# Kernel optimization log

Measured on AMD Instinct MI355X. Metric: run time of the kernel, lower is better.

## Reference

```python
import jax, jax.numpy as jnp
import numpy as np

NUM_HEADS = 16
NUM_KV_HEADS = 4
HEAD_DIM = 64
ROPE_BASE = 10000.0


def _rope(x, pos0):
    # x: [b, s, n, h_d]; interleaved-pair RoPE (torchtune RotaryPositionalEmbeddings)
    b, s, n, hd = x.shape
    half = hd // 2
    inv_freq = 1.0 / (ROPE_BASE ** (jnp.arange(0, hd, 2, dtype=jnp.float32) / hd))  # [half]
    t = jnp.arange(s, dtype=jnp.float32) + pos0                                      # [s]
    freqs = t[:, None] * inv_freq[None, :]                                           # [s, half]
    cos = jnp.cos(freqs)[None, :, None, :].astype(x.dtype)
    sin = jnp.sin(freqs)[None, :, None, :].astype(x.dtype)
    xr = x.reshape(b, s, n, half, 2)
    x1, x2 = xr[..., 0], xr[..., 1]
    o1 = x1 * cos - x2 * sin
    o2 = x1 * sin + x2 * cos
    return jnp.stack([o1, o2], axis=-1).reshape(b, s, n, hd)


def setup_inputs() -> dict:
    key = jax.random.key(0)
    k1, k2, k3 = jax.random.split(key, 3)
    b, s, d = 2, 2048, 1024
    qkv_dim = (NUM_HEADS + 2 * NUM_KV_HEADS) * HEAD_DIM  # 1536
    x = jax.random.normal(k1, (b, s, d), dtype=jnp.float32)
    Wqkv = jax.random.normal(k2, (d, qkv_dim), dtype=jnp.float32) * (d ** -0.5)
    Wo = jax.random.normal(k3, (d, d), dtype=jnp.float32) * (d ** -0.5)
    return {"x": x, "Wqkv": Wqkv, "Wo": Wo, "curr_pos": 0}


def reference(x, Wqkv, Wo, curr_pos):
    b, s, d = x.shape
    n_h, n_kv, hd = NUM_HEADS, NUM_KV_HEADS, HEAD_DIM
    q_per_kv = n_h // n_kv
    total_qkv = q_per_kv + 2

    # fused QKV projection then split per kv group
    qkv = (x @ Wqkv).reshape(b, s, n_kv, total_qkv, hd)
    q = qkv[:, :, :, :q_per_kv]            # [b, s, n_kv, q_per_kv, hd]
    k = qkv[:, :, :, q_per_kv:q_per_kv + 1]  # [b, s, n_kv, 1, hd]
    v = qkv[:, :, :, q_per_kv + 1:]          # [b, s, n_kv, 1, hd]

    # GQA expand k/v to match query heads, then flatten heads
    k = jnp.broadcast_to(k, (b, s, n_kv, q_per_kv, hd))
    v = jnp.broadcast_to(v, (b, s, n_kv, q_per_kv, hd))
    q = q.reshape(b, s, n_h, hd)
    k = k.reshape(b, s, n_h, hd)
    v = v.reshape(b, s, n_h, hd)

    # RoPE on q and k
    q = _rope(q, curr_pos)
    k = _rope(k, curr_pos)

    # causal SDPA (kv_cache is None -> is_causal=True, mask=None, dropout=0)
    scale = 1.0 / jnp.sqrt(jnp.asarray(hd, dtype=x.dtype))
    scores = jnp.einsum('bqhd,bkhd->bhqk', q, k) * scale  # [b, n_h, s, s]
    causal = jnp.tril(jnp.ones((s, s), dtype=bool))
    scores = jnp.where(causal[None, None], scores, jnp.finfo(scores.dtype).min)
    attn = jax.nn.softmax(scores, axis=-1)
    out = jnp.einsum('bhqk,bkhd->bqhd', attn, v).reshape(b, s, n_h * hd)
    return out @ Wo
```

## Files before the change

kernel.cpp:

```cpp
#include <hip/hip_runtime.h>
#include <hip/hip_bf16.h>

typedef __attribute__((ext_vector_type(8))) short bf16x8;
typedef __attribute__((ext_vector_type(4))) short bf16x4;
typedef __attribute__((ext_vector_type(4))) float f32x4;
typedef __attribute__((ext_vector_type(16))) float f32x16;
typedef unsigned short u16;
typedef unsigned int u32;

#define NH 16
#define NKV 4
#define HD 64
#define BB 2
#define SS 2048
#define DD 1024
#define QKVD 1536

#define QSCALE 0.18033688011112f
#define MBIAS  -12.0f

template<int V> struct IntC { static constexpr int value = V; };

__device__ __forceinline__ u16 f2b(float f){
  __hip_bfloat16 h = __float2bfloat16(f);
  u16 u; __builtin_memcpy(&u, &h, 2); return u;
}
__device__ __forceinline__ float b2f(u32 u){
  u <<= 16; float f; __builtin_memcpy(&f, &u, 4); return f;
}
__device__ __forceinline__ float exp2fast(float x){
#if __has_builtin(__builtin_amdgcn_exp2f)
  return __builtin_amdgcn_exp2f(x);
#else
  return exp2f(x);
#endif
}

__device__ __forceinline__ void gload16(const void* g, void* l){
  __builtin_amdgcn_global_load_lds((const __attribute__((address_space(1))) void*)g,
                                   (__attribute__((address_space(3))) void*)l, 16, 0, 0);
}

__global__ __launch_bounds__(256) void prep1(const float* __restrict__ x,
                                             u16* __restrict__ Xb,
                                             const float* __restrict__ Wqkv,
                                             u16* __restrict__ WqkvT,
                                             const float* __restrict__ Wo,
                                             u16* __restrict__ WoT){
  __shared__ u16 tile[64][65];
  const int bid = blockIdx.x;
  if (bid < 4096){
    int idx = (bid * 256 + threadIdx.x) * 4;
    float4 v = *(const float4*)(x + idx);
    u32 lo = (u32)f2b(v.x) | ((u32)f2b(v.y) << 16);
    u32 hi = (u32)f2b(v.z) | ((u32)f2b(v.w) << 16);
    *(uint2*)(Xb + idx) = make_uint2(lo, hi);
    return;
  }
  const float* in; u16* outT; int K, N, n0, k0;
  if (bid < 4480){
    int id = bid - 4096; in = Wqkv; outT = WqkvT; K = 1024; N = 1536;
    n0 = (id % 24) * 64; k0 = (id / 24) * 64;
  } else {
    int id = bid - 4480; in = Wo; outT = WoT; K = 1024; N = 1024;
    n0 = (id % 16) * 64; k0 = (id / 16) * 64;
  }
  int cr = threadIdx.x >> 6, cc = threadIdx.x & 63;
#pragma unroll
  for (int rr = 0; rr < 16; rr++){
    int row = rr * 4 + cr;
    tile[row][cc] = f2b(in[(size_t)(k0 + row) * N + n0 + cc]);
  }
  __syncthreads();
#pragma unroll
  for (int rr = 0; rr < 16; rr++){
    int row = rr * 4 + cr;
    outT[(size_t)(n0 + row) * K + k0 + cc] = tile[cc][row];
  }
}

template<int TN, typename OT>
__global__ __launch_bounds__(256) void gemm_db(const __hip_bfloat16* __restrict__ A,
                                               const __hip_bfloat16* __restrict__ BT,
                                               OT* __restrict__ C,
                                               int M, int N, int K){
  constexpr int NW = TN / 32;
  constexpr int ABYTES = 128 * 128;
  constexpr int BBYTES = TN * 128;
  __shared__ __align__(16) char smem[2][ABYTES + BBYTES];
  const int ntn = N / TN;
  int bid = blockIdx.x;
  const int cpx = gridDim.x >> 3;
  bid = (bid & 7) * cpx + (bid >> 3);
  const int tm = bid / ntn, tn = bid % ntn;
  const int m0 = tm << 7, n0 = tn * TN;
  const int lane = threadIdx.x & 63, w = threadIdx.x >> 6;
  const int g = lane >> 4, i = lane & 15;
  const int wr = w >> 1, wc = w & 1;
  f32x4 acc[4][NW] = {};
  const int lrow = lane >> 3;
  const int lcol = ((lane & 7) ^ lrow) * 8;
  const __hip_bfloat16* ga = A  + (size_t)(m0 + w * 32 + lrow) * K + lcol;
  const __hip_bfloat16* gb = BT + (size_t)(n0 + w * 8 + lrow) * K + lcol;
  const int xr = (i & 7) << 4;

  auto stage = [&](int buf, int kt){
    char* As = smem[buf];
    char* Bs = As + ABYTES;
#pragma unroll
    for (int h = 0; h < 4; h++)
      gload16(ga + kt + (size_t)(h * 8) * K, As + w * 4096 + h * 1024);
#pragma unroll
    for (int h = 0; h < NW; h++)
      gload16(gb + kt + (size_t)(h * 32) * K, Bs + (h * 4 + w) * 1024);
  };

  stage(0, 0);
  asm volatile("s_waitcnt vmcnt(0)");
  __syncthreads();
  int cur = 0;
  for (int kt = 0; kt < K; kt += 64){
    if (kt + 64 < K) stage(cur ^ 1, kt + 64);
    const char* As = smem[cur];
    const char* Bs = As + ABYTES;
    bf16x8 af[2][4], bfr[2][NW];
#pragma unroll
    for (int kh = 0; kh < 2; kh++){
#pragma unroll
      for (int x = 0; x < 4; x++)
        af[kh][x] = *(const bf16x8*)(As + (wr * 64 + x * 16 + i) * 128 + ((kh * 64 + g * 16) ^ xr));
#pragma unroll
      for (int n = 0; n < NW; n++)
        bfr[kh][n] = *(const bf16x8*)(Bs + (wc * (TN / 2) + n * 16 + i) * 128 + ((kh * 64 + g * 16) ^ xr));
    }
    __builtin_amdgcn_s_setprio(1);
#pragma unroll
    for (int kh = 0; kh < 2; kh++)
#pragma unroll
      for (int mi = 0; mi < 4; mi++)
#pragma unroll
        for (int ni = 0; ni < NW; ni++)
          acc[mi][ni] = __builtin_amdgcn_mfma_f32_16x16x32_bf16(af[kh][mi], bfr[kh][ni], acc[mi][ni], 0, 0, 0);
    __builtin_amdgcn_s_setprio(0);
    asm volatile("s_waitcnt vmcnt(0)");
    __syncthreads();
    cur ^= 1;
  }
#pragma unroll
  for (int mi = 0; mi < 4; mi++)
#pragma unroll
    for (int ni = 0; ni < NW; ni++){
      size_t base = (size_t)(m0 + wr * 64 + mi * 16 + g * 4) * N + n0 + wc * (TN / 2) + ni * 16 + i;
#pragma unroll
      for (int r = 0; r < 4; r++){
        float v = acc[mi][ni][r];
        if constexpr (sizeof(OT) == 2) C[base + (size_t)r * N] = (OT)f2b(v);
        else                           C[base + (size_t)r * N] = v;
      }
    }
}

__global__ __launch_bounds__(256) void prep2(const u16* __restrict__ qkv,
                                             const int* __restrict__ posp,
                                             u16* __restrict__ Qr,
                                             u16* __restrict__ Kr,
                                             u16* __restrict__ Vt){
  __shared__ u16 tile[64][65];
  const int bid = blockIdx.x;
  if (bid < 10240){
    int bx = bid & 255, h20 = (bid >> 8) % 20, bi = bid / 5120;
    int t = bx * 256 + threadIdx.x;
    int p = t & 31, si = t >> 5;
    int kvh = h20 / 5, slot = h20 - kvh * 5;
    const u16* src = qkv + (size_t)(bi * SS + si) * QKVD + (kvh * 6 + slot) * 64 + 2 * p;
    u32 pair = *(const u32*)src;
    float x1 = b2f(pair & 0xffffu), x2 = b2f(pair >> 16);
    int pos0 = posp[0];
    float inv_freq = exp2fast(-(float)p * 0.4152410118609203f);
    float ang = (float)(si + pos0) * inv_freq;
    float sn, cs;
    sincosf(ang, &sn, &cs);
    float o1 = x1 * cs - x2 * sn;
    float o2 = x1 * sn + x2 * cs;
    u16* dst;
    if (slot == 4){
      dst = Kr + ((size_t)(bi * NKV + kvh) * SS + si) * 64 + 2 * p;
    } else {
      o1 *= QSCALE; o2 *= QSCALE;
      dst = Qr + ((size_t)(bi * NH + kvh * 4 + slot) * SS + si) * 64 + 2 * p;
    }
    *(u32*)dst = (u32)f2b(o1) | ((u32)f2b(o2) << 16);
    return;
  }
  int id2 = bid - 10240;
  int st0 = (id2 & 31) * 64;
  int bkv = id2 >> 5;
  int bi = bkv >> 2, kvh = bkv & 3;
  int cr = threadIdx.x >> 6, cc = threadIdx.x & 63;
  const u16* src = qkv + (size_t)(bi * SS + st0) * QKVD + (kvh * 6 + 5) * 64;
#pragma unroll
  for (int rr = 0; rr < 16; rr++){
    int row = rr * 4 + cr;
    tile[row][cc] = src[(size_t)row * QKVD + cc];
  }
  __syncthreads();
  u16* dst = Vt + (size_t)bkv * 64 * SS + st0;
#pragma unroll
  for (int rr = 0; rr < 16; rr++){
    int row = rr * 4 + cr;
    dst[(size_t)row * SS + cc] = tile[cc][row];
  }
}

__global__ __launch_bounds__(256) void attn_fwd(const __hip_bfloat16* __restrict__ Qr,
                                                const __hip_bfloat16* __restrict__ Kr,
                                                const __hip_bfloat16* __restrict__ Vt,
                                                u16* __restrict__ Ao){
  __shared__ __align__(16) char smem[2][16384];
  const int blk = blockIdx.x;
  const int qt = 15 - (blk >> 5);
  const int bh = blk & 31;
  const int hi = bh & 15;
  const int bi = bh >> 4;
  const int kvh = hi >> 2;
  const int tid = threadIdx.x;
  const int lane = tid & 63, w = tid >> 6;
  const int qr = lane & 31, hlf = lane >> 5;
  const int q0 = qt * 128 + w * 32;
  const int qabs = q0 + qr;
  const u16* Qp = (const u16*)Qr + (size_t)(bi * NH + hi) * SS * 64;
  const u16* Kp = (const u16*)Kr + (size_t)(bi * NKV + kvh) * SS * 64;
  const u16* Vp = (const u16*)Vt + (size_t)(bi * NKV + kvh) * 64 * SS;

  bf16x8 qb[4];
#pragma unroll
  for (int ks = 0; ks < 4; ks++)
    qb[ks] = *(const bf16x8*)(Qp + (size_t)(q0 + qr) * 64 + ks * 16 + hlf * 8);

  const int srow = tid >> 3;
  const int sw   = ((tid & 7) ^ (srow & 7)) * 8;
  const int xr   = (lane & 7) << 4;

  auto stage = [&](int buf, int j0){
#pragma unroll
    for (int n = 0; n < 2; n++)
      gload16(Kp + (size_t)(j0 + n * 32 + srow) * 64 + sw,
              &smem[buf][n * 4096 + tid * 16]);
#pragma unroll
    for (int n = 0; n < 2; n++)
      gload16(Vp + (size_t)(n * 32 + srow) * SS + j0 + sw,
              &smem[buf][8192 + n * 4096 + tid * 16]);
  };

  float l_row = 0.f;
  f32x16 o[2] = {};

  auto body = [&](auto modec, int buf, int j0){
    constexpr int MODE = decltype(modec)::value;
    if constexpr (MODE == 2){ if (w < 2) return; }
    const bool msk = (MODE == 1) ? (w < 2) : (MODE == 2);
    const char* Kb = smem[buf];
    const char* Vb = Kb + 8192;
    f32x16 st[2];
    __builtin_amdgcn_s_setprio(1);
#pragma unroll
    for (int jb = 0; jb < 2; jb++){
      f32x16 a = {MBIAS, MBIAS, MBIAS, MBIAS, MBIAS, MBIAS, MBIAS, MBIAS,
                  MBIAS, MBIAS, MBIAS, MBIAS, MBIAS, MBIAS, MBIAS, MBIAS};
      const int row = jb * 32 + qr;
#pragma unroll
      for (int ks = 0; ks < 4; ks++){
        bf16x8 kf = *(const bf16x8*)(Kb + row * 128 + ((ks * 32 + hlf * 16) ^ xr));
        a = __builtin_amdgcn_mfma_f32_32x32x16_bf16(kf, qb[ks], a, 0, 0, 0);
      }
      st[jb] = a;
    }
    __builtin_amdgcn_s_setprio(0);
    bf16x8 vA[2][4];
#pragma unroll
    for (int db = 0; db < 2; db++){
      const int row = db * 32 + qr;
#pragma unroll
      for (int ks = 0; ks < 4; ks++)
        vA[db][ks] = *(const bf16x8*)(Vb + row * 128 + ((ks * 32 + hlf * 16) ^ xr));
    }
    float lsum = 0.f;
#pragma unroll
    for (int jb = 0; jb < 2; jb++){
      float p[16];
#pragma unroll
      for (int r = 0; r < 16; r++){
        float e = exp2fast(st[jb][r]);
        if (msk){
          int jabs = j0 + jb * 32 + (r & 3) + 8 * (r >> 2) + 4 * hlf;
          e = (jabs > qabs) ? 0.f : e;
        }
        p[r] = e;
        lsum += e;
      }
      u32 c[8];
#pragma unroll
      for (int m = 0; m < 8; m++)
        asm("v_cvt_pk_bf16_f32 %0, %1, %2" : "=v"(c[m]) : "v"(p[2 * m]), "v"(p[2 * m + 1]));
      asm volatile("v_permlane32_swap_b32 %0, %1" : "+v"(c[0]), "+v"(c[2]));
      asm volatile("v_permlane32_swap_b32 %0, %1" : "+v"(c[1]), "+v"(c[3]));
      asm volatile("v_permlane32_swap_b32 %0, %1" : "+v"(c[4]), "+v"(c[6]));
      asm volatile("v_permlane32_swap_b32 %0, %1" : "+v"(c[5]), "+v"(c[7]));
      bf16x8 pfE, pfO;
      __builtin_memcpy(&pfE, &c[0], 16);
      __builtin_memcpy(&pfO, &c[4], 16);
      __builtin_amdgcn_s_setprio(1);
#pragma unroll
      for (int db = 0; db < 2; db++){
        o[db] = __builtin_amdgcn_mfma_f32_32x32x16_bf16(vA[db][jb * 2 + 0], pfE, o[db], 0, 0, 0);
        o[db] = __builtin_amdgcn_mfma_f32_32x32x16_bf16(vA[db][jb * 2 + 1], pfO, o[db], 0, 0, 0);
      }
      __builtin_amdgcn_s_setprio(0);
    }
    lsum += __shfl_xor(lsum, 32, 64);
    l_row += lsum;
  };

  stage(0, 0);
  asm volatile("s_waitcnt vmcnt(0)");
  __syncthreads();
  int cur = 0;
  const int nfull = 2 * qt;
  for (int t = 0; t < nfull; t++){
    stage(cur ^ 1, (t + 1) * 64);
    body(IntC<0>{}, cur, t * 64);
    asm volatile("s_waitcnt vmcnt(0)");
    __syncthreads();
    cur ^= 1;
  }
  stage(cur ^ 1, (nfull + 1) * 64);
  body(IntC<1>{}, cur, nfull * 64);
  asm volatile("s_waitcnt vmcnt(0)");
  __syncthreads();
  cur ^= 1;
  body(IntC<2>{}, cur, (nfull + 1) * 64);

  const float linv = 1.f / l_row;
  u16* orow = Ao + (size_t)(bi * SS + q0 + qr) * (NH * HD) + hi * 64 + hlf * 4;
#pragma unroll
  for (int db = 0; db < 2; db++)
#pragma unroll
    for (int tg = 0; tg < 4; tg++){
      bf16x4 ov;
#pragma unroll
      for (int r = 0; r < 4; r++) ov[r] = (short)f2b(o[db][tg * 4 + r] * linv);
      *(bf16x4*)(orow + db * 32 + tg * 8) = ov;
    }
}

extern "C" void kernel_launch(void* const* d_in, const int* in_sizes, int n_in,
                              void* d_out, int out_size, void* d_ws, size_t ws_size,
                              hipStream_t stream){
  const float* x    = (const float*)d_in[0];
  const float* Wqkv = (const float*)d_in[1];
  const float* Wo   = (const float*)d_in[2];
  const int*   pos  = (const int*)d_in[3];
  float* out = (float*)d_out;
  char* ws = (char*)d_ws;

  __hip_bfloat16* Xb    = (__hip_bfloat16*)(ws);
  __hip_bfloat16* WqkvT = (__hip_bfloat16*)(ws + 8388608);
  __hip_bfloat16* WoT   = (__hip_bfloat16*)(ws + 11534336);
  u16*            QKVb  = (u16*)(ws + 13631488);
  __hip_bfloat16* Qr    = (__hip_bfloat16*)(ws + 26214400);
  __hip_bfloat16* Kr    = (__hip_bfloat16*)(ws + 34603008);
  __hip_bfloat16* Vt    = (__hip_bfloat16*)(ws + 36700160);
  __hip_bfloat16* Ao    = (__hip_bfloat16*)(ws);

  prep1<<<4736, 256, 0, stream>>>(x, (u16*)Xb, Wqkv, (u16*)WqkvT, Wo, (u16*)WoT);
  gemm_db<96, u16><<<512, 256, 0, stream>>>(Xb, WqkvT, QKVb, 4096, 1536, 1024);
  prep2<<<10496, 256, 0, stream>>>(QKVb, pos, (u16*)Qr, (u16*)Kr, (u16*)Vt);
  attn_fwd<<<512, 256, 0, stream>>>(Qr, Kr, Vt, (u16*)Ao);
  gemm_db<64, float><<<512, 256, 0, stream>>>(Ao, WoT, out, 4096, 1024, 1024);
}
```

Before: 84.21 us.

## Fuse RoPE, scaling and V transpose into the QKV GEMM epilogue

Removes the separate prep2 kernel and the bf16 QKV intermediate buffer. A new 128x128-tile QKV GEMM applies RoPE and the Q scale in its epilogue and writes V already transposed. To make the rotation pairs land in the same thread, prep1 permutes the Q/K columns of the transposed Wqkv so that even and odd elements of each pair sit 32 columns apart. This saves a kernel launch and a full read/write round trip of QKV. In exchange, the epilogue does per-element sincos and issues scattered 4-byte stores, and the grid shrinks to 384 blocks.

```diff
diff --git a/kernel.cpp b/kernel.cpp
--- a/kernel.cpp
+++ b/kernel.cpp
@@ -58,9 +58,11 @@
     return;
   }
   const float* in; u16* outT; int K, N, n0, k0;
+  bool perm = false;
   if (bid < 4480){
     int id = bid - 4096; in = Wqkv; outT = WqkvT; K = 1024; N = 1536;
     n0 = (id % 24) * 64; k0 = (id / 24) * 64;
+    perm = ((n0 >> 6) % 6) != 5;
   } else {
     int id = bid - 4480; in = Wo; outT = WoT; K = 1024; N = 1024;
     n0 = (id % 16) * 64; k0 = (id / 16) * 64;
@@ -74,8 +76,116 @@
   __syncthreads();
 #pragma unroll
   for (int rr = 0; rr < 16; rr++){
-    int row = rr * 4 + cr;
-    outT[(size_t)(n0 + row) * K + k0 + cc] = tile[cc][row];
+    int d = rr * 4 + cr;
+    int dn = perm ? ((d & 1) ? 32 + (d >> 1) : (d >> 1)) : d;
+    outT[(size_t)(n0 + dn) * K + k0 + cc] = tile[cc][d];
+  }
+}
+
+__global__ __launch_bounds__(256) void gemm_qkv(const __hip_bfloat16* __restrict__ A,
+                                                const __hip_bfloat16* __restrict__ BT,
+                                                const int* __restrict__ posp,
+                                                u16* __restrict__ Qr,
+                                                u16* __restrict__ Kr,
+                                                u16* __restrict__ Vt){
+  constexpr int Kd = 1024, N = 1536;
+  __shared__ __align__(16) char smem[2][32768];
+  int bid = blockIdx.x;
+  const int cpx = gridDim.x >> 3;
+  bid = (bid & 7) * cpx + (bid >> 3);
+  const int ntn = N >> 7;
+  const int tm = bid / ntn, tn = bid % ntn;
+  const int m0 = tm << 7, n0 = tn << 7;
+  const int lane = threadIdx.x & 63, w = threadIdx.x >> 6;
+  const int g = lane >> 4, i = lane & 15;
+  const int wr = w >> 1, wc = w & 1;
+  f32x4 acc[4][4] = {};
+  const int lrow = lane >> 3;
+  const int lcol = ((lane & 7) ^ lrow) * 8;
+  const __hip_bfloat16* ga = A  + (size_t)(m0 + w * 32 + lrow) * Kd + lcol;
+  const __hip_bfloat16* gb = BT + (size_t)(n0 + w * 32 + lrow) * Kd + lcol;
+  const int xr = (i & 7) << 4;
+
+  auto stage = [&](int buf, int kt){
+    char* As = smem[buf];
+    char* Bs = As + 16384;
+#pragma unroll
+    for (int h = 0; h < 4; h++)
+      gload16(ga + kt + (size_t)(h * 8) * Kd, As + w * 4096 + h * 1024);
+#pragma unroll
+    for (int h = 0; h < 4; h++)
+      gload16(gb + kt + (size_t)(h * 8) * Kd, Bs + w * 4096 + h * 1024);
+  };
+
+  stage(0, 0);
+  asm volatile("s_waitcnt vmcnt(0)");
+  __syncthreads();
+  int cur = 0;
+  for (int kt = 0; kt < Kd; kt += 64){
+    if (kt + 64 < Kd) stage(cur ^ 1, kt + 64);
+    const char* As = smem[cur];
+    const char* Bs = As + 16384;
+    bf16x8 af[2][4], bfr[2][4];
+#pragma unroll
+    for (int kh = 0; kh < 2; kh++){
+#pragma unroll
+      for (int x = 0; x < 4; x++){
+        af[kh][x]  = *(const bf16x8*)(As + (wr * 64 + x * 16 + i) * 128 + ((kh * 64 + g * 16) ^ xr));
+        bfr[kh][x] = *(const bf16x8*)(Bs + (wc * 64 + x * 16 + i) * 128 + ((kh * 64 + g * 16) ^ xr));
+      }
+    }
+    __builtin_amdgcn_s_setprio(1);
+#pragma unroll
+    for (int kh = 0; kh < 2; kh++)
+#pragma unroll
+      for (int mi = 0; mi < 4; mi++)
+#pragma unroll
+        for (int ni = 0; ni < 4; ni++)
+          acc[mi][ni] = __builtin_amdgcn_mfma_f32_16x16x32_bf16(af[kh][mi], bfr[kh][ni], acc[mi][ni], 0, 0, 0);
+    __builtin_amdgcn_s_setprio(0);
+    asm volatile("s_waitcnt vmcnt(0)");
+    __syncthreads();
+    cur ^= 1;
+  }
+
+  const int h24 = tn * 2 + wc;
+  const int kvh = h24 / 6, slot = h24 - kvh * 6;
+  const int bi = m0 >> 11;
+  const int s0 = (m0 & 2047) + wr * 64 + g * 4;
+  if (slot == 5){
+    u16* vb = Vt + (size_t)(bi * NKV + kvh) * 64 * SS;
+#pragma unroll
+    for (int mi = 0; mi < 4; mi++)
+#pragma unroll
+      for (int ni = 0; ni < 4; ni++){
+        bf16x4 ov;
+#pragma unroll
+        for (int r = 0; r < 4; r++) ov[r] = (short)f2b(acc[mi][ni][r]);
+        *(bf16x4*)(vb + (size_t)(ni * 16 + i) * SS + s0 + mi * 16) = ov;
+      }
+  } else {
+    const bool isq = slot < 4;
+    u16* dst0 = isq ? Qr + (size_t)(bi * NH + kvh * 4 + slot) * SS * 64
+                    : Kr + (size_t)(bi * NKV + kvh) * SS * 64;
+    const float scale = isq ? QSCALE : 1.f;
+    const int pos0 = posp[0];
+#pragma unroll
+    for (int nn = 0; nn < 2; nn++){
+      const int p = nn * 16 + i;
+      const float invf = exp2fast(-(float)p * 0.4152410118609203f);
+#pragma unroll
+      for (int mi = 0; mi < 4; mi++)
+#pragma unroll
+        for (int r = 0; r < 4; r++){
+          const int si = s0 + mi * 16 + r;
+          float sn, cs;
+          sincosf((float)(si + pos0) * invf, &sn, &cs);
+          const float x1 = acc[mi][nn][r], x2 = acc[mi][nn + 2][r];
+          const float o1 = (x1 * cs - x2 * sn) * scale;
+          const float o2 = (x1 * sn + x2 * cs) * scale;
+          *(u32*)(dst0 + (size_t)si * 64 + 2 * p) = (u32)f2b(o1) | ((u32)f2b(o2) << 16);
+        }
+    }
   }
 }
 
@@ -160,58 +270,6 @@
     }
 }
 
-__global__ __launch_bounds__(256) void prep2(const u16* __restrict__ qkv,
-                                             const int* __restrict__ posp,
-                                             u16* __restrict__ Qr,
-                                             u16* __restrict__ Kr,
-                                             u16* __restrict__ Vt){
-  __shared__ u16 tile[64][65];
-  const int bid = blockIdx.x;
-  if (bid < 10240){
-    int bx = bid & 255, h20 = (bid >> 8) % 20, bi = bid / 5120;
-    int t = bx * 256 + threadIdx.x;
-    int p = t & 31, si = t >> 5;
-    int kvh = h20 / 5, slot = h20 - kvh * 5;
-    const u16* src = qkv + (size_t)(bi * SS + si) * QKVD + (kvh * 6 + slot) * 64 + 2 * p;
-    u32 pair = *(const u32*)src;
-    float x1 = b2f(pair & 0xffffu), x2 = b2f(pair >> 16);
-    int pos0 = posp[0];
-    float inv_freq = exp2fast(-(float)p * 0.4152410118609203f);
-    float ang = (float)(si + pos0) * inv_freq;
-    float sn, cs;
-    sincosf(ang, &sn, &cs);
-    float o1 = x1 * cs - x2 * sn;
-    float o2 = x1 * sn + x2 * cs;
-    u16* dst;
-    if (slot == 4){
-      dst = Kr + ((size_t)(bi * NKV + kvh) * SS + si) * 64 + 2 * p;
-    } else {
-      o1 *= QSCALE; o2 *= QSCALE;
-      dst = Qr + ((size_t)(bi * NH + kvh * 4 + slot) * SS + si) * 64 + 2 * p;
-    }
-    *(u32*)dst = (u32)f2b(o1) | ((u32)f2b(o2) << 16);
-    return;
-  }
-  int id2 = bid - 10240;
-  int st0 = (id2 & 31) * 64;
-  int bkv = id2 >> 5;
-  int bi = bkv >> 2, kvh = bkv & 3;
-  int cr = threadIdx.x >> 6, cc = threadIdx.x & 63;
-  const u16* src = qkv + (size_t)(bi * SS + st0) * QKVD + (kvh * 6 + 5) * 64;
-#pragma unroll
-  for (int rr = 0; rr < 16; rr++){
-    int row = rr * 4 + cr;
-    tile[row][cc] = src[(size_t)row * QKVD + cc];
-  }
-  __syncthreads();
-  u16* dst = Vt + (size_t)bkv * 64 * SS + st0;
-#pragma unroll
-  for (int rr = 0; rr < 16; rr++){
-    int row = rr * 4 + cr;
-    dst[(size_t)row * SS + cc] = tile[cc][row];
-  }
-}
-
 __global__ __launch_bounds__(256) void attn_fwd(const __hip_bfloat16* __restrict__ Qr,
                                                 const __hip_bfloat16* __restrict__ Kr,
                                                 const __hip_bfloat16* __restrict__ Vt,
@@ -366,15 +424,13 @@
   __hip_bfloat16* Xb    = (__hip_bfloat16*)(ws);
   __hip_bfloat16* WqkvT = (__hip_bfloat16*)(ws + 8388608);
   __hip_bfloat16* WoT   = (__hip_bfloat16*)(ws + 11534336);
-  u16*            QKVb  = (u16*)(ws + 13631488);
   __hip_bfloat16* Qr    = (__hip_bfloat16*)(ws + 26214400);
   __hip_bfloat16* Kr    = (__hip_bfloat16*)(ws + 34603008);
   __hip_bfloat16* Vt    = (__hip_bfloat16*)(ws + 36700160);
   __hip_bfloat16* Ao    = (__hip_bfloat16*)(ws);
 
   prep1<<<4736, 256, 0, stream>>>(x, (u16*)Xb, Wqkv, (u16*)WqkvT, Wo, (u16*)WoT);
-  gemm_db<96, u16><<<512, 256, 0, stream>>>(Xb, WqkvT, QKVb, 4096, 1536, 1024);
-  prep2<<<10496, 256, 0, stream>>>(QKVb, pos, (u16*)Qr, (u16*)Kr, (u16*)Vt);
+  gemm_qkv<<<384, 256, 0, stream>>>(Xb, WqkvT, pos, (u16*)Qr, (u16*)Kr, (u16*)Vt);
   attn_fwd<<<512, 256, 0, stream>>>(Qr, Kr, Vt, (u16*)Ao);
   gemm_db<64, float><<<512, 256, 0, stream>>>(Ao, WoT, out, 4096, 1024, 1024);
 }
```

New measurement: 82.27 us. -2.3%, faster.
